# Kernel optimization log

Hardware: AMD Instinct MI355X
Metric: run time of the kernel (lower is better)

Reference implementation:

```python
import jax, jax.numpy as jnp
import numpy as np

N = 80000   # active voxels
G = 64      # voxel grid side
K = 27      # 3x3x3 kernel taps


def _build_coord_maps():
    """Random unique voxel coords in a G^3 grid; 27-tap neighbor index map (-1 = missing)."""
    rng = np.random.default_rng(0)
    flat = rng.choice(G ** 3, size=N, replace=False).astype(np.int64)
    coords = np.stack(np.unravel_index(flat, (G, G, G)), axis=1)  # (N,3)
    order = np.argsort(flat)
    skeys = flat[order]
    offs = [(dx, dy, dz) for dx in (-1, 0, 1) for dy in (-1, 0, 1) for dz in (-1, 0, 1)]
    nbr = np.full((K, N), -1, np.int32)
    for k, (dx, dy, dz) in enumerate(offs):
        nc = coords + np.array([dx, dy, dz])
        inb = np.all((nc >= 0) & (nc < G), axis=1)
        nkey = nc[:, 0] * G * G + nc[:, 1] * G + nc[:, 2]
        pos = np.clip(np.searchsorted(skeys, nkey), 0, N - 1)
        hit = inb & (skeys[pos] == nkey)
        nbr[k] = np.where(hit, order[pos], -1)
    return nbr


_W_SPECS = [('a1w', (27, 96, 64)), ('a2w', (64, 64)), ('a3w', (27, 64, 64)), ('a4w', (64, 64)),
            ('b1w', (27, 256, 64)), ('b2w', (64, 64)), ('b3w', (27, 64, 32)), ('b4w', (32, 32)),
            ('c1w', (27, 96, 128)), ('c2w', (128, 128)), ('c3w', (128, 128))]
_BN_SPECS = [('a1', 64), ('a2', 64), ('a3', 64), ('a4', 64),
             ('b1', 64), ('b2', 64), ('b3', 32), ('b4', 32),
             ('c1', 128), ('c2', 128), ('c3', 128)]


def setup_inputs() -> dict:
    key = jax.random.key(0)
    ks = jax.random.split(key, 64)
    inp = {
        'feat3d': jax.random.normal(ks[0], (N, 96), jnp.float32),
        'feat2d': jax.random.normal(ks[1], (N, 256), jnp.float32),
    }
    i = 2
    for name, shp in _W_SPECS:
        fan = float(np.prod(shp[:-1]))
        inp[name] = jax.random.normal(ks[i], shp, jnp.float32) * (1.0 / np.sqrt(fan))
        i += 1
    for pre, c in _BN_SPECS:  # folded eval-mode BN: y = x*scale + shift
        inp[pre + 's'] = 1.0 + 0.1 * jax.random.normal(ks[i], (c,), jnp.float32)
        inp[pre + 'b'] = 0.1 * jax.random.normal(ks[i + 1], (c,), jnp.float32)
        i += 2
    inp['nbr_idx'] = jnp.asarray(_build_coord_maps())
    inp['align_idx'] = jnp.arange(N, dtype=jnp.int32)  # 2D/3D share coordinates -> exact match
    return inp


def _sconv(x, W, nbr):
    """Sparse 3x3x3 conv: per-tap masked gather + GEMM, accumulated (gather-GEMM-scatter)."""
    out = jnp.zeros((x.shape[0], W.shape[-1]), x.dtype)
    for k in range(W.shape[0]):
        idx = nbr[k]
        g = jnp.where((idx >= 0)[:, None], x[jnp.maximum(idx, 0)], 0.0)
        out = out + g @ W[k]
    return out


def _bnrelu(x, s, b):
    return jax.nn.relu(x * s + b)


def reference(feat3d, feat2d,
              a1w, a2w, a3w, a4w, b1w, b2w, b3w, b4w, c1w, c2w, c3w,
              a1s, a1b, a2s, a2b, a3s, a3b, a4s, a4b,
              b1s, b1b, b2s, b2b, b3s, b3b, b4s, b4b,
              c1s, c1b, c2s, c2b, c3s, c3b,
              nbr_idx, align_idx):
    # 3D branch: 96 -> 64 (dropout = identity in eval)
    x = _bnrelu(_sconv(feat3d, a1w, nbr_idx), a1s, a1b)
    x = _bnrelu(x @ a2w, a2s, a2b)
    x = _bnrelu(_sconv(x, a3w, nbr_idx), a3s, a3b)
    x3 = _bnrelu(x @ a4w, a4s, a4b)
    # 2D branch: 256 -> 32
    y = _bnrelu(_sconv(feat2d, b1w, nbr_idx), b1s, b1b)
    y = _bnrelu(y @ b2w, b2s, b2b)
    y = _bnrelu(_sconv(y, b3w, nbr_idx), b3s, b3b)
    y2 = _bnrelu(y @ b4w, b4s, b4b)
    # features_at_coordinates: exact-match gather at the 3D coords, NaN/Inf -> 0
    ya = y2[align_idx]
    ya = jnp.where(jnp.isfinite(ya), ya, 0.0)
    # fusion: concat 64+32=96 -> 128
    z = jnp.concatenate([x3, ya], axis=1)
    z = _bnrelu(_sconv(z, c1w, nbr_idx), c1s, c1b)
    z = _bnrelu(z @ c2w, c2s, c2b)
    z = _bnrelu(z @ c3w, c3s, c3b)
    return z
```

## Files before the change

### kernel.cpp

```cpp
#include <hip/hip_runtime.h>

typedef __bf16 bf16;
typedef __bf16 bf16x8 __attribute__((ext_vector_type(8)));
typedef __bf16 bf16x4 __attribute__((ext_vector_type(4)));
typedef float  f32x4  __attribute__((ext_vector_type(4)));

__global__ void f2b_kernel(const float* __restrict__ src, bf16* __restrict__ dst, int n4) {
    int i = blockIdx.x * 256 + threadIdx.x;
    if (i >= n4) return;
    float4 v = ((const float4*)src)[i];
    bf16x4 o = { (bf16)v.x, (bf16)v.y, (bf16)v.z, (bf16)v.w };
    ((bf16x4*)dst)[i] = o;
}

__global__ void swz_kernel(const float* __restrict__ W, bf16* __restrict__ Wf,
                           int cin, int cout, int total) {
    int e = blockIdx.x * 256 + threadIdx.x;
    if (e >= total) return;
    int per_tap = cin * cout;
    int tap = e / per_tap;
    int t2  = e - tap * per_tap;
    int ntc = cout >> 4;
    int s   = t2 / (ntc * 512);
    int r3  = t2 - s * (ntc * 512);
    int nt  = r3 >> 9;
    int L   = (r3 & 511) >> 3;
    int j   = r3 & 7;
    int k   = s * 32 + (L >> 4) * 8 + j;
    int col = nt * 16 + (L & 15);
    Wf[e] = (bf16)W[((size_t)tap * cin + k) * cout + col];
}

template<int CIN, int C1, int TAPS, int KTILE, int C2, int C3>
__global__ __launch_bounds__(256) void layer_kernel(
    const bf16* __restrict__ X,
    const bf16* __restrict__ W1,
    const bf16* __restrict__ W2,
    const bf16* __restrict__ W3,
    const int*  __restrict__ nbr,
    const float* __restrict__ sc1, const float* __restrict__ sh1,
    const float* __restrict__ sc2, const float* __restrict__ sh2,
    const float* __restrict__ sc3, const float* __restrict__ sh3,
    bf16* __restrict__ Y, float* __restrict__ Yf,
    int ystride, int yoff, int n, int nblocks)
{
    constexpr int NT1  = C1 / 16;
    constexpr int KH   = CIN / KTILE;
    constexpr int KS   = KTILE / 32;
    constexpr int CH   = KTILE / 8;
    constexpr int SREG = KTILE / 32;
    constexpr int AST  = KTILE + 8;
    constexpr int WR1  = (C1 >= 64) ? 2 : 1;
    constexpr int WC1  = (C1 == 128) ? 4 : 2;
    constexpr int RG1  = 4 / WR1;
    constexpr int ABUF = 64 * AST;
    constexpr int ABY  = 2 * ABUF * 2;
    constexpr int LS1  = C1 + 8;
    constexpr int LS2  = C2 + 8;
    constexpr int L1BY = 64 * LS1 * 2;
    constexpr int L2BY = (C3 > 0) ? 64 * LS2 * 2 : 0;
    constexpr int SBY  = (ABY > L1BY ? (ABY > L2BY ? ABY : L2BY)
                                     : (L1BY > L2BY ? L1BY : L2BY));

    __shared__ __align__(16) char smem[SBY];
    __shared__ int idxs[TAPS * 64];
    bf16* As = (bf16*)smem;

    const int tid = threadIdx.x;

    {
    }
    const int bq  = nblocks >> 3, br = nblocks & 7;
    const int bx  = blockIdx.x & 7, bs = blockIdx.x >> 3;
    const int sb  = bx * bq + (bx < br ? bx : br) + bs;
    const int base = sb * 64;

    const int lane  = tid & 63;
    const int wv    = tid >> 6;
    const int m16   = lane & 15;
    const int quad  = lane >> 4;
    const int wrow1 = wv % RG1;
    const int wcol1 = wv / RG1;

    for (int e = tid; e < TAPS * 64; e += 256)
        idxs[e] = nbr[(e >> 6) * n + base + (e & 63)];
    __syncthreads();

    int rr[SREG], cof[SREG], lofs[SREG];
#pragma unroll
    for (int j = 0; j < SREG; ++j) {
        int e = tid + 256 * j;
        rr[j]   = e / CH;
        int c   = e - rr[j] * CH;
        cof[j]  = c * 8;
        lofs[j] = rr[j] * AST + c * 8;
    }

    float4 sreg[SREG];
    auto issue_loads = [&](int kh, int t) {
#pragma unroll
        for (int j = 0; j < SREG; ++j) {
            int idx = idxs[t * 64 + rr[j]];
            float4 val = {0.f, 0.f, 0.f, 0.f};
            if (idx >= 0) val = *(const float4*)(X + (size_t)idx * CIN + kh * KTILE + cof[j]);
            sreg[j] = val;
        }
    };
    auto store_lds = [&](int buf) {
#pragma unroll
        for (int j = 0; j < SREG; ++j)
            *(float4*)(&As[buf * ABUF + lofs[j]]) = sreg[j];
    };

    f32x4 acc1[WR1][WC1];
#pragma unroll
    for (int r = 0; r < WR1; ++r)
#pragma unroll
        for (int c = 0; c < WC1; ++c) acc1[r][c] = (f32x4){0.f, 0.f, 0.f, 0.f};

    issue_loads(0, 0);
    store_lds(0);

    int it = 0;
    for (int kh = 0; kh < KH; ++kh)
        for (int t = 0; t < TAPS; ++t, ++it) {
            __syncthreads();

            const bf16* wt = W1 + (size_t)t * (CIN * C1);
            bf16x8 bfr[KS][WC1];
#pragma unroll
            for (int s = 0; s < KS; ++s)
#pragma unroll
                for (int c = 0; c < WC1; ++c)
                    bfr[s][c] = *(const bf16x8*)(wt + ((kh * KS + s) * NT1 + wcol1 * WC1 + c) * 512 + lane * 8);

            int t2 = t + 1, kh2 = kh;
            if (t2 == TAPS) { t2 = 0; kh2 = kh + 1; }
            const bool more = (kh2 < KH);
            if (more) issue_loads(kh2, t2);

            const int buf = it & 1;
#pragma unroll
            for (int s = 0; s < KS; ++s) {
                bf16x8 a[WR1];
#pragma unroll
                for (int r = 0; r < WR1; ++r)
                    a[r] = *(const bf16x8*)(&As[buf * ABUF + ((wrow1 * WR1 + r) * 16 + m16) * AST + s * 32 + quad * 8]);
#pragma unroll
                for (int r = 0; r < WR1; ++r)
#pragma unroll
                    for (int c = 0; c < WC1; ++c)
                        acc1[r][c] = __builtin_amdgcn_mfma_f32_16x16x32_bf16(a[r], bfr[s][c], acc1[r][c], 0, 0, 0);
            }

            if (more) store_lds(buf ^ 1);
        }

    __syncthreads();
    bf16* Lt1 = (bf16*)smem;
#pragma unroll
    for (int c = 0; c < WC1; ++c) {
        int col = (wcol1 * WC1 + c) * 16 + m16;
        float s1 = sc1[col], h1 = sh1[col];
#pragma unroll
        for (int r = 0; r < WR1; ++r) {
            int row0 = (wrow1 * WR1 + r) * 16 + quad * 4;
#pragma unroll
            for (int i = 0; i < 4; ++i) {
                float v = acc1[r][c][i] * s1 + h1;
                v = v > 0.f ? v : 0.f;
                Lt1[(row0 + i) * LS1 + col] = (bf16)v;
            }
        }
    }
    __syncthreads();

    constexpr int NT2 = C2 / 16;
    constexpr int WR2 = (C2 >= 64) ? 2 : 1;
    constexpr int WC2 = (C2 == 128) ? 4 : 2;
    constexpr int RG2 = 4 / WR2;
    constexpr int KS2 = C1 / 32;
    const int wrow2 = wv % RG2, wcol2 = wv / RG2;

    f32x4 acc2[WR2][WC2];
#pragma unroll
    for (int r = 0; r < WR2; ++r)
#pragma unroll
        for (int c = 0; c < WC2; ++c) acc2[r][c] = (f32x4){0.f, 0.f, 0.f, 0.f};

#pragma unroll
    for (int s = 0; s < KS2; ++s) {
        bf16x8 a[WR2], bw[WC2];
#pragma unroll
        for (int r = 0; r < WR2; ++r)
            a[r] = *(const bf16x8*)(&Lt1[((wrow2 * WR2 + r) * 16 + m16) * LS1 + s * 32 + quad * 8]);
#pragma unroll
        for (int c = 0; c < WC2; ++c)
            bw[c] = *(const bf16x8*)(W2 + ((s * NT2 + wcol2 * WC2 + c) * 512 + lane * 8));
#pragma unroll
        for (int r = 0; r < WR2; ++r)
#pragma unroll
            for (int c = 0; c < WC2; ++c)
                acc2[r][c] = __builtin_amdgcn_mfma_f32_16x16x32_bf16(a[r], bw[c], acc2[r][c], 0, 0, 0);
    }

    if constexpr (C3 == 0) {
#pragma unroll
        for (int c = 0; c < WC2; ++c) {
            int col = (wcol2 * WC2 + c) * 16 + m16;
            float s2 = sc2[col], h2 = sh2[col];
#pragma unroll
            for (int r = 0; r < WR2; ++r) {
                int row0 = base + (wrow2 * WR2 + r) * 16 + quad * 4;
#pragma unroll
                for (int i = 0; i < 4; ++i) {
                    float v = acc2[r][c][i] * s2 + h2;
                    v = v > 0.f ? v : 0.f;
                    size_t off = (size_t)(row0 + i) * ystride + yoff + col;
                    if (Yf) Yf[off] = v;
                    else    Y[off] = (bf16)v;
                }
            }
        }
    } else {
        __syncthreads();
        bf16* Lt2 = (bf16*)smem;
#pragma unroll
        for (int c = 0; c < WC2; ++c) {
            int col = (wcol2 * WC2 + c) * 16 + m16;
            float s2 = sc2[col], h2 = sh2[col];
#pragma unroll
            for (int r = 0; r < WR2; ++r) {
                int row0 = (wrow2 * WR2 + r) * 16 + quad * 4;
#pragma unroll
                for (int i = 0; i < 4; ++i) {
                    float v = acc2[r][c][i] * s2 + h2;
                    v = v > 0.f ? v : 0.f;
                    Lt2[(row0 + i) * LS2 + col] = (bf16)v;
                }
            }
        }
        __syncthreads();

        constexpr int C3v = (C3 > 0) ? C3 : 16;
        constexpr int NT3 = C3v / 16;
        constexpr int WR3 = (C3v >= 64) ? 2 : 1;
        constexpr int WC3 = (C3v == 128) ? 4 : 2;
        constexpr int RG3 = 4 / WR3;
        constexpr int KS3 = C2 / 32;
        const int wrow3 = wv % RG3, wcol3 = wv / RG3;

        f32x4 acc3[WR3][WC3];
#pragma unroll
        for (int r = 0; r < WR3; ++r)
#pragma unroll
            for (int c = 0; c < WC3; ++c) acc3[r][c] = (f32x4){0.f, 0.f, 0.f, 0.f};

#pragma unroll
        for (int s = 0; s < KS3; ++s) {
            bf16x8 a[WR3], bw[WC3];
#pragma unroll
            for (int r = 0; r < WR3; ++r)
                a[r] = *(const bf16x8*)(&Lt2[((wrow3 * WR3 + r) * 16 + m16) * LS2 + s * 32 + quad * 8]);
#pragma unroll
            for (int c = 0; c < WC3; ++c)
                bw[c] = *(const bf16x8*)(W3 + ((s * NT3 + wcol3 * WC3 + c) * 512 + lane * 8));
#pragma unroll
            for (int r = 0; r < WR3; ++r)
#pragma unroll
                for (int c = 0; c < WC3; ++c)
                    acc3[r][c] = __builtin_amdgcn_mfma_f32_16x16x32_bf16(a[r], bw[c], acc3[r][c], 0, 0, 0);
        }

#pragma unroll
        for (int c = 0; c < WC3; ++c) {
            int col = (wcol3 * WC3 + c) * 16 + m16;
            float s3 = sc3[col], h3 = sh3[col];
#pragma unroll
            for (int r = 0; r < WR3; ++r) {
                int row0 = base + (wrow3 * WR3 + r) * 16 + quad * 4;
#pragma unroll
                for (int i = 0; i < 4; ++i) {
                    float v = acc3[r][c][i] * s3 + h3;
                    v = v > 0.f ? v : 0.f;
                    size_t off = (size_t)(row0 + i) * ystride + yoff + col;
                    if (Yf) Yf[off] = v;
                    else    Y[off] = (bf16)v;
                }
            }
        }
    }
}

__global__ void concat_kernel(const bf16* __restrict__ y2, const int* __restrict__ align,
                              bf16* __restrict__ z, int n) {
    int e = blockIdx.x * 256 + threadIdx.x;
    if (e >= n * 32) return;
    int i = e >> 5, c = e & 31;
    int a = align[i];
    float v = (float)y2[(size_t)a * 32 + c];
    unsigned u = __builtin_bit_cast(unsigned, v);
    if ((u & 0x7f800000u) == 0x7f800000u) v = 0.f;
    z[(size_t)i * 96 + 64 + c] = (bf16)v;
}

extern "C" void kernel_launch(void* const* d_in, const int* in_sizes, int n_in,
                              void* d_out, int out_size, void* d_ws, size_t ws_size,
                              hipStream_t stream) {
    const float* feat3d = (const float*)d_in[0];
    const float* feat2d = (const float*)d_in[1];
    const float* Wsrc[11];
    for (int i = 0; i < 11; ++i) Wsrc[i] = (const float*)d_in[2 + i];
    const float* bn[22];
    for (int i = 0; i < 22; ++i) bn[i] = (const float*)d_in[13 + i];
    const int* nbr   = (const int*)d_in[35];
    const int* align = (const int*)d_in[36];
    float* out = (float*)d_out;

    const int n = in_sizes[0] / 96;

    char* ws = (char*)d_ws;
    size_t off = 0;
    auto alloc = [&](size_t bytes) -> void* {
        void* p = ws + off;
        off = (off + bytes + 255) & ~(size_t)255;
        return p;
    };
    bf16* F3 = (bf16*)alloc((size_t)n * 96 * 2);
    bf16* F2 = (bf16*)alloc((size_t)n * 256 * 2);
    static const int wt_taps[11] = {27, 1, 27, 1, 27, 1, 27, 1, 27, 1, 1};
    static const int wt_cin[11]  = {96, 64, 64, 64, 256, 64, 64, 32, 96, 128, 128};
    static const int wt_cout[11] = {64, 64, 64, 64, 64, 64, 32, 32, 128, 128, 128};
    bf16* Wf[11];
    for (int i = 0; i < 11; ++i)
        Wf[i] = (bf16*)alloc((size_t)wt_taps[i] * wt_cin[i] * wt_cout[i] * 2);
    bf16* tA = (bf16*)alloc((size_t)n * 64 * 2);
    bf16* tB = (bf16*)alloc((size_t)n * 64 * 2);
    bf16* y2 = (bf16*)alloc((size_t)n * 32 * 2);
    bf16* z  = (bf16*)alloc((size_t)n * 96 * 2);

    f2b_kernel<<<(n * 96 / 4 + 255) / 256, 256, 0, stream>>>(feat3d, F3, n * 96 / 4);
    f2b_kernel<<<(n * 256 / 4 + 255) / 256, 256, 0, stream>>>(feat2d, F2, n * 256 / 4);
    for (int i = 0; i < 11; ++i) {
        int total = wt_taps[i] * wt_cin[i] * wt_cout[i];
        swz_kernel<<<(total + 255) / 256, 256, 0, stream>>>(Wsrc[i], Wf[i], wt_cin[i], wt_cout[i], total);
    }

    const int GB = n / 64;

    layer_kernel<96, 64, 27, 96, 64, 0><<<GB, 256, 0, stream>>>(
        F3, Wf[0], Wf[1], nullptr, nbr,
        bn[0], bn[1], bn[2], bn[3], nullptr, nullptr,
        tB, nullptr, 64, 0, n, GB);
    layer_kernel<64, 64, 27, 64, 64, 0><<<GB, 256, 0, stream>>>(
        tB, Wf[2], Wf[3], nullptr, nbr,
        bn[4], bn[5], bn[6], bn[7], nullptr, nullptr,
        z, nullptr, 96, 0, n, GB);

    layer_kernel<256, 64, 27, 128, 64, 0><<<GB, 256, 0, stream>>>(
        F2, Wf[4], Wf[5], nullptr, nbr,
        bn[8], bn[9], bn[10], bn[11], nullptr, nullptr,
        tA, nullptr, 64, 0, n, GB);
    layer_kernel<64, 32, 27, 64, 32, 0><<<GB, 256, 0, stream>>>(
        tA, Wf[6], Wf[7], nullptr, nbr,
        bn[12], bn[13], bn[14], bn[15], nullptr, nullptr,
        y2, nullptr, 32, 0, n, GB);

    concat_kernel<<<(n * 32 + 255) / 256, 256, 0, stream>>>(y2, align, z, n);

    layer_kernel<96, 128, 27, 96, 128, 128><<<GB, 256, 0, stream>>>(
        z, Wf[8], Wf[9], Wf[10], nbr,
        bn[16], bn[17], bn[18], bn[19], bn[20], bn[21],
        nullptr, out, 128, 0, n, GB);
}
```

Baseline: 592.1 us.

## Enlarge sparse-conv row tile to 128 voxels with 4x row-tiles per wave

After: 592.1 us. About the same (-0.0%).

```diff
diff --git a/kernel.cpp b/kernel.cpp
--- a/kernel.cpp
+++ b/kernel.cpp
@@ -32,7 +32,7 @@
 }
 
 template<int CIN, int C1, int TAPS, int KTILE, int C2, int C3>
-__global__ __launch_bounds__(256) void layer_kernel(
+__global__ __launch_bounds__(256, 3) void layer_kernel(
     const bf16* __restrict__ X,
     const bf16* __restrict__ W1,
     const bf16* __restrict__ W2,
@@ -44,46 +44,44 @@
     bf16* __restrict__ Y, float* __restrict__ Yf,
     int ystride, int yoff, int n, int nblocks)
 {
+    constexpr int M    = 128;
     constexpr int NT1  = C1 / 16;
+    constexpr int WR1  = 4;
+    constexpr int WC1  = (NT1 >= 2) ? NT1 / 2 : 1;
     constexpr int KH   = CIN / KTILE;
     constexpr int KS   = KTILE / 32;
     constexpr int CH   = KTILE / 8;
-    constexpr int SREG = KTILE / 32;
+    constexpr int SREG = KTILE / 16;
     constexpr int AST  = KTILE + 8;
-    constexpr int WR1  = (C1 >= 64) ? 2 : 1;
-    constexpr int WC1  = (C1 == 128) ? 4 : 2;
-    constexpr int RG1  = 4 / WR1;
-    constexpr int ABUF = 64 * AST;
+    constexpr int ABUF = M * AST;
     constexpr int ABY  = 2 * ABUF * 2;
     constexpr int LS1  = C1 + 8;
     constexpr int LS2  = C2 + 8;
-    constexpr int L1BY = 64 * LS1 * 2;
-    constexpr int L2BY = (C3 > 0) ? 64 * LS2 * 2 : 0;
+    constexpr int L1BY = M * LS1 * 2;
+    constexpr int L2BY = (C3 > 0) ? M * LS2 * 2 : 0;
     constexpr int SBY  = (ABY > L1BY ? (ABY > L2BY ? ABY : L2BY)
                                      : (L1BY > L2BY ? L1BY : L2BY));
 
     __shared__ __align__(16) char smem[SBY];
-    __shared__ int idxs[TAPS * 64];
+    __shared__ int idxs[TAPS * M];
     bf16* As = (bf16*)smem;
 
     const int tid = threadIdx.x;
 
-    {
-    }
     const int bq  = nblocks >> 3, br = nblocks & 7;
     const int bx  = blockIdx.x & 7, bs = blockIdx.x >> 3;
     const int sb  = bx * bq + (bx < br ? bx : br) + bs;
-    const int base = sb * 64;
+    const int base = sb * M;
 
     const int lane  = tid & 63;
     const int wv    = tid >> 6;
     const int m16   = lane & 15;
     const int quad  = lane >> 4;
-    const int wrow1 = wv % RG1;
-    const int wcol1 = wv / RG1;
-
-    for (int e = tid; e < TAPS * 64; e += 256)
-        idxs[e] = nbr[(e >> 6) * n + base + (e & 63)];
+    const int wrow1 = wv & 1;
+    const int wcol1 = wv >> 1;
+
+    for (int e = tid; e < TAPS * M; e += 256)
+        idxs[e] = nbr[(e >> 7) * n + base + (e & (M - 1))];
     __syncthreads();
 
     int rr[SREG], cof[SREG], lofs[SREG];
@@ -100,7 +98,7 @@
     auto issue_loads = [&](int kh, int t) {
 #pragma unroll
         for (int j = 0; j < SREG; ++j) {
-            int idx = idxs[t * 64 + rr[j]];
+            int idx = idxs[t * M + rr[j]];
             float4 val = {0.f, 0.f, 0.f, 0.f};
             if (idx >= 0) val = *(const float4*)(X + (size_t)idx * CIN + kh * KTILE + cof[j]);
             sreg[j] = val;
@@ -176,11 +174,10 @@
     __syncthreads();
 
     constexpr int NT2 = C2 / 16;
-    constexpr int WR2 = (C2 >= 64) ? 2 : 1;
-    constexpr int WC2 = (C2 == 128) ? 4 : 2;
-    constexpr int RG2 = 4 / WR2;
+    constexpr int WR2 = 4;
+    constexpr int WC2 = (NT2 >= 2) ? NT2 / 2 : 1;
     constexpr int KS2 = C1 / 32;
-    const int wrow2 = wv % RG2, wcol2 = wv / RG2;
+    const int wrow2 = wv & 1, wcol2 = wv >> 1;
 
     f32x4 acc2[WR2][WC2];
 #pragma unroll
@@ -244,11 +241,10 @@
 
         constexpr int C3v = (C3 > 0) ? C3 : 16;
         constexpr int NT3 = C3v / 16;
-        constexpr int WR3 = (C3v >= 64) ? 2 : 1;
-        constexpr int WC3 = (C3v == 128) ? 4 : 2;
-        constexpr int RG3 = 4 / WR3;
+        constexpr int WR3 = 4;
+        constexpr int WC3 = (NT3 >= 2) ? NT3 / 2 : 1;
         constexpr int KS3 = C2 / 32;
-        const int wrow3 = wv % RG3, wcol3 = wv / RG3;
+        const int wrow3 = wv & 1, wcol3 = wv >> 1;
 
         f32x4 acc3[WR3][WC3];
 #pragma unroll
@@ -346,9 +342,9 @@
         swz_kernel<<<(total + 255) / 256, 256, 0, stream>>>(Wsrc[i], Wf[i], wt_cin[i], wt_cout[i], total);
     }
 
-    const int GB = n / 64;
-
-    layer_kernel<96, 64, 27, 96, 64, 0><<<GB, 256, 0, stream>>>(
+    const int GB = n / 128;
+
+    layer_kernel<96, 64, 27, 32, 64, 0><<<GB, 256, 0, stream>>>(
         F3, Wf[0], Wf[1], nullptr, nbr,
         bn[0], bn[1], bn[2], bn[3], nullptr, nullptr,
         tB, nullptr, 64, 0, n, GB);
@@ -357,7 +353,7 @@
         bn[4], bn[5], bn[6], bn[7], nullptr, nullptr,
         z, nullptr, 96, 0, n, GB);
 
-    layer_kernel<256, 64, 27, 128, 64, 0><<<GB, 256, 0, stream>>>(
+    layer_kernel<256, 64, 27, 64, 64, 0><<<GB, 256, 0, stream>>>(
         F2, Wf[4], Wf[5], nullptr, nbr,
         bn[8], bn[9], bn[10], bn[11], nullptr, nullptr,
         tA, nullptr, 64, 0, n, GB);
@@ -368,7 +364,7 @@
 
     concat_kernel<<<(n * 32 + 255) / 256, 256, 0, stream>>>(y2, align, z, n);
 
-    layer_kernel<96, 128, 27, 96, 128, 128><<<GB, 256, 0, stream>>>(
+    layer_kernel<96, 128, 27, 32, 128, 128><<<GB, 256, 0, stream>>>(
         z, Wf[8], Wf[9], Wf[10], nbr,
         bn[16], bn[17], bn[18], bn[19], bn[20], bn[21],
         nullptr, out, 128, 0, n, GB);
```
